# Kernel tuning notes

Measured on AMD Instinct MI355X. Metric: run time of the kernel, lower is better.

The kernel has to match this reference:

```python
import jax, jax.numpy as jnp
import numpy as np

B, T, D = 8, 1024, 1024
H, HS = 16, 64  # num_heads, head_size; H*HS == D


def setup_inputs() -> dict:
    key = jax.random.key(0)
    ks = jax.random.split(key, 5)
    scale = 0.02
    x = jax.random.normal(ks[0], (B, T, D), dtype=jnp.float32)
    Wq = jax.random.normal(ks[1], (H, D, HS), dtype=jnp.float32) * scale
    Wk = jax.random.normal(ks[2], (H, D, HS), dtype=jnp.float32) * scale
    Wv = jax.random.normal(ks[3], (H, D, HS), dtype=jnp.float32) * scale
    Wo = jax.random.normal(ks[4], (D, D), dtype=jnp.float32) * scale
    bo = jnp.zeros((D,), dtype=jnp.float32)
    return {"x": x, "Wq": Wq, "Wk": Wk, "Wv": Wv, "Wo": Wo, "bo": bo}


def reference(x, Wq, Wk, Wv, Wo, bo):
    # Per-head linear projections (bias-free, as in Head): [B,H,T,HS]
    q = jnp.einsum('btd,hds->bhts', x, Wq)
    k = jnp.einsum('btd,hds->bhts', x, Wk)
    v = jnp.einsum('btd,hds->bhts', x, Wv)
    # Scaled scores with causal mask: [B,H,T,T]
    scores = jnp.einsum('bhts,bhus->bhtu', q, k) * (HS ** -0.5)
    causal = jnp.tril(jnp.ones((T, T), dtype=bool))
    scores = jnp.where(causal, scores, jnp.finfo(scores.dtype).min)
    att = jax.nn.softmax(scores, axis=-1)
    # Weighted sum over values, then concat heads: [B,T,H*HS]
    out = jnp.einsum('bhtu,bhus->bhts', att, v)
    out = out.transpose(0, 2, 1, 3).reshape(B, T, H * HS)
    # Output projection (nn.Linear: y = x @ W^T + b)
    return out @ Wo.T + bo
```

## Files before the change

### kernel.cpp

```cpp
#include <hip/hip_runtime.h>
#include <hip/hip_bf16.h>

#define BBATCH 8
#define TSEQ   1024
#define DMODEL 1024
#define NHEAD  16
#define HSZ    64

typedef unsigned short ushort_t;
typedef __attribute__((ext_vector_type(8))) short short8;
typedef __attribute__((ext_vector_type(4))) float float4v;

__device__ __forceinline__ ushort_t f2bf(float f) {
    __hip_bfloat16 h = __float2bfloat16(f);
    return *reinterpret_cast<ushort_t*>(&h);
}
__device__ __forceinline__ ushort_t f2bf_fast(float f) {
    return (ushort_t)((__float_as_uint(f) + 0x8000u) >> 16);
}
__device__ __forceinline__ unsigned int pack_bf2(float lo, float hi) {
    unsigned int a = __float_as_uint(lo) + 0x8000u;
    unsigned int b = __float_as_uint(hi) + 0x8000u;
    return __builtin_amdgcn_perm(b, a, 0x07060302u);
}

__device__ __forceinline__ short8 cvt8(const float* f) {
    union { ushort_t u[8]; short8 v; } r;
    #pragma unroll
    for (int e = 0; e < 8; ++e) r.u[e] = f2bf(f[e]);
    return r.v;
}

__device__ __forceinline__ void async16(const ushort_t* g, ushort_t* l) {
    __builtin_amdgcn_global_load_lds(
        (const __attribute__((address_space(1))) unsigned int*)g,
        (__attribute__((address_space(3))) unsigned int*)l, 16, 0, 0);
}

template<int N> __device__ __forceinline__ void vwait() {
    if constexpr (N == 3)      asm volatile("s_waitcnt vmcnt(3)" ::: "memory");
    else if constexpr (N == 0) asm volatile("s_waitcnt vmcnt(0)" ::: "memory");
}

__global__ __launch_bounds__(256) void cvt_f32_bf16(
    const float* __restrict__ src, ushort_t* __restrict__ dst)
{
    const size_t idx = ((size_t)blockIdx.x * 256 + threadIdx.x) * 16;
    float f[16];
    *(float4*)(f + 0)  = *(const float4*)(src + idx);
    *(float4*)(f + 4)  = *(const float4*)(src + idx + 4);
    *(float4*)(f + 8)  = *(const float4*)(src + idx + 8);
    *(float4*)(f + 12) = *(const float4*)(src + idx + 12);
    uint4 o0 = make_uint4(pack_bf2(f[0], f[1]),   pack_bf2(f[2], f[3]),
                          pack_bf2(f[4], f[5]),   pack_bf2(f[6], f[7]));
    uint4 o1 = make_uint4(pack_bf2(f[8], f[9]),   pack_bf2(f[10], f[11]),
                          pack_bf2(f[12], f[13]), pack_bf2(f[14], f[15]));
    *(uint4*)(dst + idx) = o0;
    *(uint4*)(dst + idx + 8) = o1;
}

__global__ __launch_bounds__(256) void pack_w(
    const float* __restrict__ Wq, const float* __restrict__ Wk,
    const float* __restrict__ Wv, ushort_t* __restrict__ WpT)
{
    __shared__ ushort_t L[64 * 72];
    const int tid = threadIdx.x;
    const int d0 = blockIdx.x * 64;
    const int wh = blockIdx.y;
    const int w = wh >> 4, h = wh & 15;
    const float* W = (w == 0 ? Wq : (w == 1 ? Wk : Wv)) + (size_t)h * DMODEL * HSZ;

    int dr = tid >> 2, sc = (tid & 3) * 16;
    const float4* src = (const float4*)(W + (size_t)(d0 + dr) * HSZ + sc);
    float f[16];
    *(float4*)(f + 0) = src[0]; *(float4*)(f + 4) = src[1];
    *(float4*)(f + 8) = src[2]; *(float4*)(f + 12) = src[3];
    *(short8*)(L + dr * 72 + sc)     = cvt8(f);
    *(short8*)(L + dr * 72 + sc + 8) = cvt8(f + 8);
    __syncthreads();

    int s = tid >> 2, dc = (tid & 3) * 16;
    union { ushort_t u[16]; short8 v[2]; } o;
    #pragma unroll
    for (int j = 0; j < 16; ++j) o.u[j] = L[(dc + j) * 72 + s];
    ushort_t* dst = WpT + (size_t)(w * 1024 + h * 64 + s) * DMODEL + d0 + dc;
    *(short8*)dst = o.v[0];
    *(short8*)(dst + 8) = o.v[1];
}

template<bool STG, int VW>
__device__ __forceinline__ void kstep32(
    const ushort_t* Ab, const ushort_t* Bb,
    ushort_t* An, ushort_t* Bn,
    const ushort_t*& gA, const ushort_t*& gB,
    const int wave,
    const int (&aoff)[4], const int (&boff)[4],
    float4v (&acc)[4][4])
{
    short8 av[4], bv[4];
    #pragma unroll
    for (int a = 0; a < 4; ++a) av[a] = *(const short8*)(Ab + aoff[a]);
    #pragma unroll
    for (int b = 0; b < 4; ++b) bv[b] = *(const short8*)(Bb + boff[b]);
    if (STG) {
        async16(gA,                  An + wave * 512);
        async16(gB,                  Bn + wave * 512);
        async16(gB + 128 * DMODEL,   Bn + 4096 + wave * 512);
        gA += 32; gB += 32;
    }
    __builtin_amdgcn_s_setprio(1);
    #pragma unroll
    for (int a = 0; a < 4; ++a)
        #pragma unroll
        for (int b = 0; b < 4; ++b)
            acc[a][b] = __builtin_amdgcn_mfma_f32_16x16x32_bf16(
                av[a], bv[b], acc[a][b], 0, 0, 0);
    __builtin_amdgcn_s_setprio(0);
    vwait<VW>();
    __builtin_amdgcn_s_barrier();
}

__global__ __launch_bounds__(512, 2) void qkv_gemm(
    const ushort_t* __restrict__ Xb, const ushort_t* __restrict__ WpT,
    ushort_t* __restrict__ Qb, ushort_t* __restrict__ Kb, ushort_t* __restrict__ Vt)
{
    __shared__ ushort_t Ab[3][128 * 32];
    __shared__ ushort_t Bb[3][256 * 32];

    const int tid = threadIdx.x;
    const int wave = tid >> 6, lane = tid & 63;
    const int q = lane >> 4, cc = lane & 15;
    const int wm = wave >> 2, wn = wave & 3;

    const int bid = blockIdx.x;
    const int xcd = bid & 7;
    const bool isV = (bid >= 512);
    int ta, tb;
    if (!isV) {
        int lo = bid >> 3;
        ta = lo >> 2;
        tb = xcd * 4 + (lo & 3);
    } else {
        int lo = (bid - 512) >> 3;
        ta = xcd * 8 + (lo & 7);
        tb = lo >> 3;
    }
    const ushort_t* pA = isV ? Xb  + (size_t)ta * 128 * DMODEL
                             : WpT + (size_t)ta * 128 * DMODEL;
    const ushort_t* pB = isV ? WpT + (size_t)(2048 + tb * 256) * DMODEL
                             : Xb  + (size_t)tb * 256 * DMODEL;

    const int srow = lane >> 2;
    const int chx = (lane & 3) ^ (srow & 3);
    const ushort_t* gA = pA + (size_t)(wave * 16 + srow) * DMODEL + chx * 8;
    const ushort_t* gB = pB + (size_t)(wave * 16 + srow) * DMODEL + chx * 8;

    int aoff[4], boff[4];
    #pragma unroll
    for (int f = 0; f < 4; ++f) {
        aoff[f] = (wm * 64 + f * 16 + cc) * 32 + ((q ^ (cc & 3)) * 8);
        boff[f] = (wn * 64 + f * 16 + cc) * 32 + ((q ^ (cc & 3)) * 8);
    }

    float4v acc[4][4];
    #pragma unroll
    for (int a = 0; a < 4; ++a)
        #pragma unroll
        for (int b = 0; b < 4; ++b) acc[a][b] = (float4v){0.f, 0.f, 0.f, 0.f};

    async16(gA,                Ab[0] + wave * 512);
    async16(gB,                Bb[0] + wave * 512);
    async16(gB + 128 * DMODEL, Bb[0] + 4096 + wave * 512);
    gA += 32; gB += 32;
    async16(gA,                Ab[1] + wave * 512);
    async16(gB,                Bb[1] + wave * 512);
    async16(gB + 128 * DMODEL, Bb[1] + 4096 + wave * 512);
    gA += 32; gB += 32;
    vwait<3>();
    __builtin_amdgcn_s_barrier();

    #pragma unroll 1
    for (int it = 0; it < 10; ++it) {
        kstep32<true, 3>(Ab[0], Bb[0], Ab[2], Bb[2], gA, gB, wave, aoff, boff, acc);
        kstep32<true, 3>(Ab[1], Bb[1], Ab[0], Bb[0], gA, gB, wave, aoff, boff, acc);
        kstep32<true, 3>(Ab[2], Bb[2], Ab[1], Bb[1], gA, gB, wave, aoff, boff, acc);
    }
    kstep32<false, 0>(Ab[0], Bb[0], Ab[2], Bb[2], gA, gB, wave, aoff, boff, acc);
    kstep32<false, -1>(Ab[1], Bb[1], Ab[0], Bb[0], gA, gB, wave, aoff, boff, acc);

    if (!isV) {
        ushort_t* Out = (ta < 8) ? Qb : Kb;
        const float osc = (ta < 8) ? 0.18033688011112042f : 1.0f;
        const int h = ((ta * 128 + wm * 64) >> 6) & 15;
        #pragma unroll
        for (int b = 0; b < 4; ++b) {
            int mc = tb * 256 + wn * 64 + b * 16 + cc;
            int bb = mc >> 10, t = mc & 1023;
            size_t rb = (((size_t)(bb * NHEAD + h)) * TSEQ + t) * HSZ;
            #pragma unroll
            for (int a = 0; a < 4; ++a) {
                int s0 = a * 16 + q * 4;
                uint2 pk = make_uint2(
                    pack_bf2(acc[a][b][0] * osc, acc[a][b][1] * osc),
                    pack_bf2(acc[a][b][2] * osc, acc[a][b][3] * osc));
                *(uint2*)(Out + rb + s0) = pk;
            }
        }
    } else {
        #pragma unroll
        for (int b = 0; b < 4; ++b) {
            int nc = tb * 256 + wn * 64 + b * 16 + cc;
            int h = nc >> 6, s = nc & 63;
            #pragma unroll
            for (int a = 0; a < 4; ++a) {
                int mr = ta * 128 + wm * 64 + a * 16 + q * 4;
                int bb = mr >> 10, t0 = mr & 1023;
                size_t addr = (((size_t)(bb * NHEAD + h)) * HSZ + s) * TSEQ + t0;
                uint2 pk = make_uint2(pack_bf2(acc[a][b][0], acc[a][b][1]),
                                      pack_bf2(acc[a][b][2], acc[a][b][3]));
                *(uint2*)(Vt + addr) = pk;
            }
        }
    }
}

__global__ __launch_bounds__(256) void attn(
    const ushort_t* __restrict__ Qb, const ushort_t* __restrict__ Kb,
    const ushort_t* __restrict__ Vt, ushort_t* __restrict__ Ob)
{
    __shared__ ushort_t Ks[2][64 * 64];
    __shared__ ushort_t VTs[2][64 * 64];
    __shared__ ushort_t Ps[4][32 * 72];
    const int tid = threadIdx.x;
    const int wave = tid >> 6, lane = tid & 63;
    const int q = lane >> 4, cc = lane & 15;
    const int bid = blockIdx.x;
    const int qt = 7 - (bid >> 7);
    const int bh = bid & 127;
    const size_t base = (size_t)bh * TSEQ * HSZ;
    const int J = 2 * qt + 2;

    const ushort_t* kg[2]; const ushort_t* vg[2]; int dmo[2];
    #pragma unroll
    for (int i = 0; i < 2; ++i) {
        int rr = wave * 16 + i * 8 + (lane >> 3);
        int ch = (lane & 7) ^ (rr & 7);
        kg[i] = Kb + base + (size_t)rr * HSZ + ch * 8;
        vg[i] = Vt + base + (size_t)rr * TSEQ + ch * 8;
        dmo[i] = (wave * 16 + i * 8) * 64;
    }

    short8 qf[2][2];
    #pragma unroll
    for (int tt = 0; tt < 2; ++tt) {
        const ushort_t* qp = Qb + base +
            (size_t)(qt * 128 + wave * 32 + tt * 16 + cc) * HSZ + q * 8;
        qf[tt][0] = *(const short8*)qp;
        qf[tt][1] = *(const short8*)(qp + 32);
    }

    int koff[4][2], poff[2][2];
    #pragma unroll
    for (int ut = 0; ut < 4; ++ut)
        #pragma unroll
        for (int kt = 0; kt < 2; ++kt)
            koff[ut][kt] = (ut * 16 + cc) * 64 + (((kt * 4 + q) ^ (cc & 7)) * 8);
    #pragma unroll
    for (int tt = 0; tt < 2; ++tt)
        #pragma unroll
        for (int kt = 0; kt < 2; ++kt)
            poff[tt][kt] = (tt * 16 + cc) * 72 + kt * 32 + q * 8;

    float4v oacc[2][4];
    #pragma unroll
    for (int tt = 0; tt < 2; ++tt)
        #pragma unroll
        for (int st = 0; st < 4; ++st) oacc[tt][st] = (float4v){0.f, 0.f, 0.f, 0.f};
    float lsum[2] = {0.f, 0.f};

    #pragma unroll
    for (int i = 0; i < 2; ++i) {
        async16(kg[i], &Ks[0][dmo[i]]);
        async16(vg[i], &VTs[0][dmo[i]]);
    }
    __syncthreads();

    for (int jt = 0; jt < J; ++jt) {
        const ushort_t* Kc = Ks[jt & 1];
        const ushort_t* Vc = VTs[jt & 1];
        if (jt + 1 < J) {
            int nb = (jt + 1) & 1;
            #pragma unroll
            for (int i = 0; i < 2; ++i) {
                async16(kg[i] + (size_t)(jt + 1) * 64 * HSZ, &Ks[nb][dmo[i]]);
                async16(vg[i] + (jt + 1) * 64, &VTs[nb][dmo[i]]);
            }
        }

        float4v sc[4][2];
        #pragma unroll
        for (int ut = 0; ut < 4; ++ut)
            #pragma unroll
            for (int tt = 0; tt < 2; ++tt) sc[ut][tt] = (float4v){0.f, 0.f, 0.f, 0.f};
        #pragma unroll
        for (int kt = 0; kt < 2; ++kt) {
            short8 kf[4];
            #pragma unroll
            for (int ut = 0; ut < 4; ++ut) kf[ut] = *(const short8*)(Kc + koff[ut][kt]);
            #pragma unroll
            for (int ut = 0; ut < 4; ++ut) {
                sc[ut][0] = __builtin_amdgcn_mfma_f32_16x16x32_bf16(
                    kf[ut], qf[0][kt], sc[ut][0], 0, 0, 0);
                sc[ut][1] = __builtin_amdgcn_mfma_f32_16x16x32_bf16(
                    kf[ut], qf[1][kt], sc[ut][1], 0, 0, 0);
            }
        }

        if ((jt >> 1) == qt) {
            #pragma unroll
            for (int tt = 0; tt < 2; ++tt) {
                const int tg = qt * 128 + wave * 32 + tt * 16 + cc;
                #pragma unroll
                for (int ut = 0; ut < 4; ++ut) {
                    float pv[4]; float ps = 0.f;
                    #pragma unroll
                    for (int rr = 0; rr < 4; ++rr) {
                        float p = exp2f(sc[ut][tt][rr]);
                        if ((jt * 64 + ut * 16 + q * 4 + rr) > tg) p = 0.f;
                        pv[rr] = p; ps += p;
                    }
                    lsum[tt] += ps;
                    *(uint2*)&Ps[wave][(tt * 16 + cc) * 72 + ut * 16 + q * 4] =
                        make_uint2(pack_bf2(pv[0], pv[1]), pack_bf2(pv[2], pv[3]));
                }
            }
        } else {
            #pragma unroll
            for (int tt = 0; tt < 2; ++tt) {
                #pragma unroll
                for (int ut = 0; ut < 4; ++ut) {
                    float pv[4]; float ps = 0.f;
                    #pragma unroll
                    for (int rr = 0; rr < 4; ++rr) {
                        float p = exp2f(sc[ut][tt][rr]);
                        pv[rr] = p; ps += p;
                    }
                    lsum[tt] += ps;
                    *(uint2*)&Ps[wave][(tt * 16 + cc) * 72 + ut * 16 + q * 4] =
                        make_uint2(pack_bf2(pv[0], pv[1]), pack_bf2(pv[2], pv[3]));
                }
            }
        }

        #pragma unroll
        for (int kt = 0; kt < 2; ++kt) {
            short8 pa0 = *(const short8*)&Ps[wave][poff[0][kt]];
            short8 pa1 = *(const short8*)&Ps[wave][poff[1][kt]];
            #pragma unroll
            for (int st = 0; st < 4; ++st) {
                short8 vf = *(const short8*)(Vc + koff[st][kt]);
                oacc[0][st] = __builtin_amdgcn_mfma_f32_16x16x32_bf16(
                    pa0, vf, oacc[0][st], 0, 0, 0);
                oacc[1][st] = __builtin_amdgcn_mfma_f32_16x16x32_bf16(
                    pa1, vf, oacc[1][st], 0, 0, 0);
            }
        }
        __syncthreads();
    }

    float inv[2];
    #pragma unroll
    for (int tt = 0; tt < 2; ++tt) {
        float l = lsum[tt];
        l += __shfl_xor(l, 16);
        l += __shfl_xor(l, 32);
        inv[tt] = 1.f / l;
    }
    const int b = bh >> 4, h = bh & 15;
    #pragma unroll
    for (int tt = 0; tt < 2; ++tt)
        #pragma unroll
        for (int rr = 0; rr < 4; ++rr) {
            float iv = __shfl(inv[tt], q * 4 + rr);
            int t = qt * 128 + wave * 32 + tt * 16 + q * 4 + rr;
            size_t rb = ((size_t)b * TSEQ + t) * DMODEL + h * HSZ;
            #pragma unroll
            for (int st = 0; st < 4; ++st)
                Ob[rb + st * 16 + cc] = f2bf_fast(oacc[tt][st][rr] * iv);
        }
}

__global__ __launch_bounds__(256) void oproj_gemm(
    const ushort_t* __restrict__ Obuf, const ushort_t* __restrict__ Wob,
    const float* __restrict__ bo, float* __restrict__ out)
{
    __shared__ ushort_t As[128 * 64];
    __shared__ ushort_t Bs[128 * 64];
    const int tid = threadIdx.x;
    const int wave = tid >> 6, lane = tid & 63;
    const int q = lane >> 4, cc = lane & 15;
    const int bid = blockIdx.x;
    const int xcd = bid & 7, local = bid >> 3;
    const int n0 = (local >> 3) * 128;
    const int m0 = (xcd * 8 + (local & 7)) * 128;
    const int wm = wave >> 1, wn = wave & 1;

    const ushort_t* ag[4]; const ushort_t* bg[4]; int lo_[4];
    #pragma unroll
    for (int i = 0; i < 4; ++i) {
        int row = wave * 32 + i * 8 + (lane >> 3);
        int ch = (lane & 7) ^ (row & 7);
        ag[i] = Obuf + (size_t)(m0 + row) * DMODEL + ch * 8;
        bg[i] = Wob + (size_t)(n0 + row) * DMODEL + ch * 8;
        lo_[i] = (wave * 32 + i * 8) * 64;
    }
    int aoff[4][2], boff[4][2];
    #pragma unroll
    for (int mt = 0; mt < 4; ++mt) {
        int row = wm * 64 + mt * 16 + cc;
        #pragma unroll
        for (int kt = 0; kt < 2; ++kt)
            aoff[mt][kt] = row * 64 + (((kt * 4 + q) ^ (row & 7)) * 8);
    }
    #pragma unroll
    for (int nt = 0; nt < 4; ++nt) {
        int row = wn * 64 + nt * 16 + cc;
        #pragma unroll
        for (int kt = 0; kt < 2; ++kt)
            boff[nt][kt] = row * 64 + (((kt * 4 + q) ^ (row & 7)) * 8);
    }

    float4v acc[4][4];
    #pragma unroll
    for (int a = 0; a < 4; ++a)
        #pragma unroll
        for (int b = 0; b < 4; ++b) acc[a][b] = (float4v){0.f, 0.f, 0.f, 0.f};

    for (int j = 0; j < 16; ++j) {
        #pragma unroll
        for (int i = 0; i < 4; ++i) {
            async16(ag[i], As + lo_[i]);
            async16(bg[i], Bs + lo_[i]);
            ag[i] += 64; bg[i] += 64;
        }
        __syncthreads();

        short8 av[4][2], bv[4][2];
        #pragma unroll
        for (int mt = 0; mt < 4; ++mt) {
            av[mt][0] = *(const short8*)(As + aoff[mt][0]);
            av[mt][1] = *(const short8*)(As + aoff[mt][1]);
        }
        #pragma unroll
        for (int nt = 0; nt < 4; ++nt) {
            bv[nt][0] = *(const short8*)(Bs + boff[nt][0]);
            bv[nt][1] = *(const short8*)(Bs + boff[nt][1]);
        }
        #pragma unroll
        for (int kt = 0; kt < 2; ++kt)
            #pragma unroll
            for (int mt = 0; mt < 4; ++mt)
                #pragma unroll
                for (int nt = 0; nt < 4; ++nt)
                    acc[mt][nt] = __builtin_amdgcn_mfma_f32_16x16x32_bf16(
                        av[mt][kt], bv[nt][kt], acc[mt][nt], 0, 0, 0);
        __syncthreads();
    }

    #pragma unroll
    for (int nt = 0; nt < 4; ++nt) {
        int n = n0 + wn * 64 + nt * 16 + cc;
        float bias = bo[n];
        #pragma unroll
        for (int mt = 0; mt < 4; ++mt)
            #pragma unroll
            for (int rr = 0; rr < 4; ++rr) {
                int m = m0 + wm * 64 + mt * 16 + q * 4 + rr;
                out[(size_t)m * DMODEL + n] = acc[mt][nt][rr] + bias;
            }
    }
}

extern "C" void kernel_launch(void* const* d_in, const int* in_sizes, int n_in,
                              void* d_out, int out_size, void* d_ws, size_t ws_size,
                              hipStream_t stream)
{
    const float* x  = (const float*)d_in[0];
    const float* Wq = (const float*)d_in[1];
    const float* Wk = (const float*)d_in[2];
    const float* Wv = (const float*)d_in[3];
    const float* Wo = (const float*)d_in[4];
    const float* bo = (const float*)d_in[5];
    float* out = (float*)d_out;

    const size_t SEG = (size_t)8 * 1024 * 1024;
    ushort_t* Qb  = (ushort_t*)d_ws;
    ushort_t* Kb  = Qb + SEG;
    ushort_t* Vtb = Kb + SEG;
    ushort_t* WpT = Vtb + SEG;
    ushort_t* Ob  = WpT;
    ushort_t* Xb  = (ushort_t*)d_out;
    ushort_t* Wob = Qb;

    cvt_f32_bf16<<<dim3(2048),    256, 0, stream>>>(x, Xb);
    pack_w      <<<dim3(16, 48),  256, 0, stream>>>(Wq, Wk, Wv, WpT);
    qkv_gemm    <<<dim3(768),     512, 0, stream>>>(Xb, WpT, Qb, Kb, Vtb);
    attn        <<<dim3(1024),    256, 0, stream>>>(Qb, Kb, Vtb, Ob);
    cvt_f32_bf16<<<dim3(256),     256, 0, stream>>>(Wo, Wob);
    oproj_gemm  <<<dim3(512),     256, 0, stream>>>(Ob, Wob, bo, out);
}
```

Baseline: 231.2 us.

## Use 4-wave blocks with 128x64 per-wave tiles in QKV GEMM

```diff
diff --git a/kernel.cpp b/kernel.cpp
--- a/kernel.cpp
+++ b/kernel.cpp
@@ -38,7 +38,8 @@
 }
 
 template<int N> __device__ __forceinline__ void vwait() {
-    if constexpr (N == 3)      asm volatile("s_waitcnt vmcnt(3)" ::: "memory");
+    if constexpr (N == 6)      asm volatile("s_waitcnt vmcnt(6)" ::: "memory");
+    else if constexpr (N == 3) asm volatile("s_waitcnt vmcnt(3)" ::: "memory");
     else if constexpr (N == 0) asm volatile("s_waitcnt vmcnt(0)" ::: "memory");
 }
 
@@ -94,23 +95,26 @@
     ushort_t* An, ushort_t* Bn,
     const ushort_t*& gA, const ushort_t*& gB,
     const int wave,
-    const int (&aoff)[4], const int (&boff)[4],
-    float4v (&acc)[4][4])
-{
-    short8 av[4], bv[4];
-    #pragma unroll
-    for (int a = 0; a < 4; ++a) av[a] = *(const short8*)(Ab + aoff[a]);
+    const int (&aoff)[8], const int (&boff)[4],
+    float4v (&acc)[8][4])
+{
+    short8 av[8], bv[4];
+    #pragma unroll
+    for (int a = 0; a < 8; ++a) av[a] = *(const short8*)(Ab + aoff[a]);
     #pragma unroll
     for (int b = 0; b < 4; ++b) bv[b] = *(const short8*)(Bb + boff[b]);
     if (STG) {
-        async16(gA,                  An + wave * 512);
-        async16(gB,                  Bn + wave * 512);
-        async16(gB + 128 * DMODEL,   Bn + 4096 + wave * 512);
+        async16(gA,                An + (wave)     * 512);
+        async16(gA + 64 * DMODEL,  An + (wave + 4) * 512);
+        async16(gB,                Bn + (wave)     * 512);
+        async16(gB + 64 * DMODEL,  Bn + (wave + 4) * 512);
+        async16(gB + 128 * DMODEL, Bn + (wave + 8) * 512);
+        async16(gB + 192 * DMODEL, Bn + (wave + 12) * 512);
         gA += 32; gB += 32;
     }
     __builtin_amdgcn_s_setprio(1);
     #pragma unroll
-    for (int a = 0; a < 4; ++a)
+    for (int a = 0; a < 8; ++a)
         #pragma unroll
         for (int b = 0; b < 4; ++b)
             acc[a][b] = __builtin_amdgcn_mfma_f32_16x16x32_bf16(
@@ -120,7 +124,7 @@
     __builtin_amdgcn_s_barrier();
 }
 
-__global__ __launch_bounds__(512, 2) void qkv_gemm(
+__global__ __launch_bounds__(256, 2) void qkv_gemm(
     const ushort_t* __restrict__ Xb, const ushort_t* __restrict__ WpT,
     ushort_t* __restrict__ Qb, ushort_t* __restrict__ Kb, ushort_t* __restrict__ Vt)
 {
@@ -130,7 +134,6 @@
     const int tid = threadIdx.x;
     const int wave = tid >> 6, lane = tid & 63;
     const int q = lane >> 4, cc = lane & 15;
-    const int wm = wave >> 2, wn = wave & 3;
 
     const int bid = blockIdx.x;
     const int xcd = bid & 7;
@@ -151,39 +154,47 @@
                              : Xb  + (size_t)tb * 256 * DMODEL;
 
     const int srow = lane >> 2;
-    const int chx = (lane & 3) ^ (srow & 3);
+    const int chx = (lane & 3) ^ ((lane >> 3) & 3);
     const ushort_t* gA = pA + (size_t)(wave * 16 + srow) * DMODEL + chx * 8;
     const ushort_t* gB = pB + (size_t)(wave * 16 + srow) * DMODEL + chx * 8;
 
-    int aoff[4], boff[4];
-    #pragma unroll
-    for (int f = 0; f < 4; ++f) {
-        aoff[f] = (wm * 64 + f * 16 + cc) * 32 + ((q ^ (cc & 3)) * 8);
-        boff[f] = (wn * 64 + f * 16 + cc) * 32 + ((q ^ (cc & 3)) * 8);
-    }
-
-    float4v acc[4][4];
-    #pragma unroll
-    for (int a = 0; a < 4; ++a)
+    int aoff[8], boff[4];
+    const int cswz = (q ^ ((cc >> 1) & 3)) * 8;
+    #pragma unroll
+    for (int f = 0; f < 8; ++f)
+        aoff[f] = (f * 16 + cc) * 32 + cswz;
+    #pragma unroll
+    for (int f = 0; f < 4; ++f)
+        boff[f] = (wave * 64 + f * 16 + cc) * 32 + cswz;
+
+    float4v acc[8][4];
+    #pragma unroll
+    for (int a = 0; a < 8; ++a)
         #pragma unroll
         for (int b = 0; b < 4; ++b) acc[a][b] = (float4v){0.f, 0.f, 0.f, 0.f};
 
-    async16(gA,                Ab[0] + wave * 512);
-    async16(gB,                Bb[0] + wave * 512);
-    async16(gB + 128 * DMODEL, Bb[0] + 4096 + wave * 512);
+    async16(gA,                Ab[0] + (wave)     * 512);
+    async16(gA + 64 * DMODEL,  Ab[0] + (wave + 4) * 512);
+    async16(gB,                Bb[0] + (wave)     * 512);
+    async16(gB + 64 * DMODEL,  Bb[0] + (wave + 4) * 512);
+    async16(gB + 128 * DMODEL, Bb[0] + (wave + 8) * 512);
+    async16(gB + 192 * DMODEL, Bb[0] + (wave + 12) * 512);
     gA += 32; gB += 32;
-    async16(gA,                Ab[1] + wave * 512);
-    async16(gB,                Bb[1] + wave * 512);
-    async16(gB + 128 * DMODEL, Bb[1] + 4096 + wave * 512);
+    async16(gA,                Ab[1] + (wave)     * 512);
+    async16(gA + 64 * DMODEL,  Ab[1] + (wave + 4) * 512);
+    async16(gB,                Bb[1] + (wave)     * 512);
+    async16(gB + 64 * DMODEL,  Bb[1] + (wave + 4) * 512);
+    async16(gB + 128 * DMODEL, Bb[1] + (wave + 8) * 512);
+    async16(gB + 192 * DMODEL, Bb[1] + (wave + 12) * 512);
     gA += 32; gB += 32;
-    vwait<3>();
+    vwait<6>();
     __builtin_amdgcn_s_barrier();
 
     #pragma unroll 1
     for (int it = 0; it < 10; ++it) {
-        kstep32<true, 3>(Ab[0], Bb[0], Ab[2], Bb[2], gA, gB, wave, aoff, boff, acc);
-        kstep32<true, 3>(Ab[1], Bb[1], Ab[0], Bb[0], gA, gB, wave, aoff, boff, acc);
-        kstep32<true, 3>(Ab[2], Bb[2], Ab[1], Bb[1], gA, gB, wave, aoff, boff, acc);
+        kstep32<true, 6>(Ab[0], Bb[0], Ab[2], Bb[2], gA, gB, wave, aoff, boff, acc);
+        kstep32<true, 6>(Ab[1], Bb[1], Ab[0], Bb[0], gA, gB, wave, aoff, boff, acc);
+        kstep32<true, 6>(Ab[2], Bb[2], Ab[1], Bb[1], gA, gB, wave, aoff, boff, acc);
     }
     kstep32<false, 0>(Ab[0], Bb[0], Ab[2], Bb[2], gA, gB, wave, aoff, boff, acc);
     kstep32<false, -1>(Ab[1], Bb[1], Ab[0], Bb[0], gA, gB, wave, aoff, boff, acc);
@@ -191,29 +202,29 @@
     if (!isV) {
         ushort_t* Out = (ta < 8) ? Qb : Kb;
         const float osc = (ta < 8) ? 0.18033688011112042f : 1.0f;
-        const int h = ((ta * 128 + wm * 64) >> 6) & 15;
         #pragma unroll
         for (int b = 0; b < 4; ++b) {
-            int mc = tb * 256 + wn * 64 + b * 16 + cc;
+            int mc = tb * 256 + wave * 64 + b * 16 + cc;
             int bb = mc >> 10, t = mc & 1023;
-            size_t rb = (((size_t)(bb * NHEAD + h)) * TSEQ + t) * HSZ;
-            #pragma unroll
-            for (int a = 0; a < 4; ++a) {
-                int s0 = a * 16 + q * 4;
+            #pragma unroll
+            for (int a = 0; a < 8; ++a) {
+                int srw = ta * 128 + a * 16 + q * 4;
+                int h = (srw >> 6) & 15, s0 = srw & 63;
+                size_t addr = (((size_t)(bb * NHEAD + h)) * TSEQ + t) * HSZ + s0;
                 uint2 pk = make_uint2(
                     pack_bf2(acc[a][b][0] * osc, acc[a][b][1] * osc),
                     pack_bf2(acc[a][b][2] * osc, acc[a][b][3] * osc));
-                *(uint2*)(Out + rb + s0) = pk;
+                *(uint2*)(Out + addr) = pk;
             }
         }
     } else {
         #pragma unroll
         for (int b = 0; b < 4; ++b) {
-            int nc = tb * 256 + wn * 64 + b * 16 + cc;
+            int nc = tb * 256 + wave * 64 + b * 16 + cc;
             int h = nc >> 6, s = nc & 63;
             #pragma unroll
-            for (int a = 0; a < 4; ++a) {
-                int mr = ta * 128 + wm * 64 + a * 16 + q * 4;
+            for (int a = 0; a < 8; ++a) {
+                int mr = ta * 128 + a * 16 + q * 4;
                 int bb = mr >> 10, t0 = mr & 1023;
                 size_t addr = (((size_t)(bb * NHEAD + h)) * HSZ + s) * TSEQ + t0;
                 uint2 pk = make_uint2(pack_bf2(acc[a][b][0], acc[a][b][1]),
@@ -504,7 +515,7 @@
 
     cvt_f32_bf16<<<dim3(2048),    256, 0, stream>>>(x, Xb);
     pack_w      <<<dim3(16, 48),  256, 0, stream>>>(Wq, Wk, Wv, WpT);
-    qkv_gemm    <<<dim3(768),     512, 0, stream>>>(Xb, WpT, Qb, Kb, Vtb);
+    qkv_gemm    <<<dim3(768),     256, 0, stream>>>(Xb, WpT, Qb, Kb, Vtb);
     attn        <<<dim3(1024),    256, 0, stream>>>(Qb, Kb, Vtb, Ob);
     cvt_f32_bf16<<<dim3(256),     256, 0, stream>>>(Wo, Wob);
     oproj_gemm  <<<dim3(512),     256, 0, stream>>>(Ob, Wob, bo, out);
```

New measurement: 223.8 us. 3.2% less time.
